# Kernel tuning notes

Measured on AMD Instinct MI355X. Metric: run time of the kernel, lower is better.

The kernel has to match this reference:

```python
import jax, jax.numpy as jnp
import numpy as np

N_HEAD = 16


def setup_inputs() -> dict:
    key = jax.random.key(0)
    k1, k2, k3 = jax.random.split(key, 3)
    B, T, C = 2, 2048, 1024
    x = jax.random.normal(k1, (B, T, C), dtype=jnp.float32)
    attention_mask = jnp.zeros((B, 1, 1, T), dtype=jnp.float32)
    W_attn = jax.random.normal(k2, (C, 3 * C), dtype=jnp.float32) * 0.02
    b_attn = jnp.zeros((3 * C,), dtype=jnp.float32)
    W_proj = jax.random.normal(k3, (C, C), dtype=jnp.float32) * 0.02
    b_proj = jnp.zeros((C,), dtype=jnp.float32)
    return {"x": x, "attention_mask": attention_mask, "W_attn": W_attn,
            "b_attn": b_attn, "W_proj": W_proj, "b_proj": b_proj}


def reference(x, attention_mask, W_attn, b_attn, W_proj, b_proj):
    B, T, C = x.shape
    H = N_HEAD
    d = C // H
    qkv = x @ W_attn + b_attn                      # [B, T, 3C]
    q, k, v = jnp.split(qkv, 3, axis=-1)
    q = q.reshape(B, T, H, d).transpose(0, 2, 1, 3)  # [B, H, T, d]
    k = k.reshape(B, T, H, d).transpose(0, 2, 1, 3)
    v = v.reshape(B, T, H, d).transpose(0, 2, 1, 3)
    att = jnp.einsum('bhtd,bhsd->bhts', q, k) * (1.0 / np.sqrt(d))
    causal = jnp.tril(jnp.ones((T, T), dtype=bool))
    att = jnp.where(causal[None, None], att, jnp.float32(-10000.0))
    att = att + attention_mask                     # additive broadcast mask
    att = jax.nn.softmax(att, axis=-1)             # dropout p=0.0 -> identity
    y = jnp.einsum('bhts,bhsd->bhtd', att, v)      # [B, H, T, d]
    y = y.transpose(0, 2, 1, 3).reshape(B, T, C)
    return y @ W_proj + b_proj
```

## Files before the change

### kernel.cpp

```cpp
#include <hip/hip_runtime.h>
#include <hip/hip_bf16.h>
#include <stdint.h>

#define BATCH 2
#define TT 2048
#define CC 1024
#define NH 16
#define HD 64

typedef __attribute__((ext_vector_type(8))) short short8;
typedef __attribute__((ext_vector_type(4))) short sh4;
typedef __attribute__((ext_vector_type(4))) float f32x4;

#define MFMA16 __builtin_amdgcn_mfma_f32_16x16x32_bf16

__device__ __forceinline__ short f2bf(float f) {
  union { float f; unsigned u; } x;
  x.f = f;
  unsigned r = x.u + 0x7FFFu + ((x.u >> 16) & 1u);
  return (short)(r >> 16);
}

__global__ __launch_bounds__(256) void cast_f32_bf16(
    const float* __restrict__ s, short* __restrict__ d, int n) {
  const int i = (blockIdx.x * 256 + threadIdx.x) * 8;
  if (i >= n) return;
  const float4 a = *reinterpret_cast<const float4*>(&s[i]);
  const float4 b = *reinterpret_cast<const float4*>(&s[i + 4]);
  short8 o;
  o[0] = f2bf(a.x); o[1] = f2bf(a.y); o[2] = f2bf(a.z); o[3] = f2bf(a.w);
  o[4] = f2bf(b.x); o[5] = f2bf(b.y); o[6] = f2bf(b.z); o[7] = f2bf(b.w);
  *reinterpret_cast<short8*>(&d[i]) = o;
}

__global__ __launch_bounds__(256) void transpose_cast_bf16(
    const float* __restrict__ W, short* __restrict__ Wt, int K, int N) {
  __shared__ __align__(16) float Ls[64][68];
  const int n0 = blockIdx.x * 64, k0 = blockIdx.y * 64;
  const int tid = threadIdx.x;
  {
    const int r = tid >> 4, c4 = (tid & 15) * 4;
#pragma unroll
    for (int p = 0; p < 4; ++p) {
      const float4 v = *reinterpret_cast<const float4*>(
          &W[(size_t)(k0 + r + p * 16) * N + n0 + c4]);
      *reinterpret_cast<float4*>(&Ls[r + p * 16][c4]) = v;
    }
  }
  __syncthreads();
  {
    const int n = tid >> 2;
    const int kk0 = (tid & 3) * 16;
#pragma unroll
    for (int half = 0; half < 2; ++half) {
      short8 o;
#pragma unroll
      for (int t = 0; t < 8; ++t) o[t] = f2bf(Ls[kk0 + half * 8 + t][n]);
      *reinterpret_cast<short8*>(&Wt[(size_t)(n0 + n) * K + k0 + kk0 + half * 8]) = o;
    }
  }
}

__global__ __launch_bounds__(256) void transpose_v(
    const short* __restrict__ qkv, short* __restrict__ vT) {
  __shared__ __align__(16) short Ls[64][72];
  const int s0 = blockIdx.x * 64;
  const int bh = blockIdx.y, b = bh >> 4, h = bh & 15;
  const int tid = threadIdx.x;
  const int r = tid >> 3, c = (tid & 7) * 8;
#pragma unroll
  for (int p = 0; p < 2; ++p) {
    *reinterpret_cast<short8*>(&Ls[r + p * 32][c]) =
        *reinterpret_cast<const short8*>(
            &qkv[(size_t)(b * TT + s0 + r + p * 32) * (3 * CC) + 2 * CC +
                 h * HD + c]);
  }
  __syncthreads();
  const int d = tid >> 2, ss = (tid & 3) * 16;
  short8 o0, o1;
#pragma unroll
  for (int t = 0; t < 8; ++t) { o0[t] = Ls[ss + t][d]; o1[t] = Ls[ss + 8 + t][d]; }
  short* dst = &vT[((size_t)(bh * HD + d)) * TT + s0 + ss];
  *reinterpret_cast<short8*>(dst) = o0;
  *reinterpret_cast<short8*>(dst + 8) = o1;
}

template <bool OUT_BF16>
__global__ __launch_bounds__(256) void gemm_bt_mfma(
    const short* __restrict__ A, const short* __restrict__ Bt,
    const float* __restrict__ bias, void* __restrict__ C, int M, int N, int K,
    int QS) {
  __shared__ __align__(16) short As[2 * 128 * 32];
  __shared__ __align__(16) short Bs[2 * 128 * 32];
  const int tid = threadIdx.x;
  const int w = tid >> 6, lane = tid & 63;
  const int quad = lane >> 4, l15 = lane & 15;
  const int m0 = blockIdx.y * 128, n0 = blockIdx.x * 128;
  const int wm = (w >> 1) * 64, wn = (w & 1) * 64;

  f32x4 acc[4][4] = {};
  const int row16 = lane >> 2;
  const int c4 = (lane & 3) * 8;

  for (int k0 = 0; k0 < K; k0 += 64) {
    __syncthreads();
#pragma unroll
    for (int p = 0; p < 2; ++p) {
      const int rbase = __builtin_amdgcn_readfirstlane((w * 2 + p) * 16);
#pragma unroll
      for (int kh = 0; kh < 2; ++kh) {
        const short* ga = &A[(size_t)(m0 + rbase + row16) * K + k0 + kh * 32 + c4];
        const short* gb = &Bt[(size_t)(n0 + rbase + row16) * K + k0 + kh * 32 + c4];
        __builtin_amdgcn_global_load_lds(
            (const __attribute__((address_space(1))) void*)ga,
            (__attribute__((address_space(3))) void*)&As[kh * 4096 + rbase * 32],
            16, 0, 0);
        __builtin_amdgcn_global_load_lds(
            (const __attribute__((address_space(1))) void*)gb,
            (__attribute__((address_space(3))) void*)&Bs[kh * 4096 + rbase * 32],
            16, 0, 0);
      }
    }
    __syncthreads();

    short8 af[2][4], bfr[2][4];
#pragma unroll
    for (int kh = 0; kh < 2; ++kh) {
#pragma unroll
      for (int i = 0; i < 4; ++i)
        af[kh][i] = *reinterpret_cast<const short8*>(
            &As[kh * 4096 + (wm + i * 16 + l15) * 32 + quad * 8]);
#pragma unroll
      for (int j = 0; j < 4; ++j)
        bfr[kh][j] = *reinterpret_cast<const short8*>(
            &Bs[kh * 4096 + (wn + j * 16 + l15) * 32 + quad * 8]);
    }
#pragma unroll
    for (int kh = 0; kh < 2; ++kh)
#pragma unroll
      for (int i = 0; i < 4; ++i)
#pragma unroll
        for (int j = 0; j < 4; ++j)
          acc[i][j] = MFMA16(af[kh][i], bfr[kh][j], acc[i][j], 0, 0, 0);
  }

#pragma unroll
  for (int i = 0; i < 4; ++i) {
#pragma unroll
    for (int r = 0; r < 4; ++r) {
      const int row = m0 + wm + i * 16 + quad * 4 + r;
#pragma unroll
      for (int j = 0; j < 4; ++j) {
        const int col = n0 + wn + j * 16 + l15;
        float v = acc[i][j][r] + bias[col];
        if (col < QS) v *= 0.125f;
        if (OUT_BF16)
          ((short*)C)[(size_t)row * N + col] = f2bf(v);
        else
          ((float*)C)[(size_t)row * N + col] = v;
      }
    }
  }
}

#define PST 72
__global__ __launch_bounds__(512) void attn_mfma5(
    const short* __restrict__ qkv, const short* __restrict__ vT,
    const float* __restrict__ mask, short* __restrict__ y) {
  __shared__ __align__(16) short Ks[2][64 * PST];
  __shared__ __align__(16) short Vs[2][64 * PST];
  __shared__ __align__(16) short Ps[128 * PST];
  const int tid = threadIdx.x;
  const int w = tid >> 6, lane = tid & 63;
  const int quad = lane >> 4, l15 = lane & 15;
  const int bh = blockIdx.y, b = bh >> 4, h = bh & 15;
  const int px = blockIdx.x;
  const int qh = 15 - px;
  const int nth = 2 * qh + 2;
  const int ntl = 2 * px + 2;
  const int ntot = nth + ntl;
  const int RS = 3 * CC;

  int qrow0 = qh * 128 + w * 16;

  short8 qf0, qf1;
  {
    const size_t qrow = (size_t)(b * TT + qrow0 + l15) * RS + h * HD + quad * 8;
    qf0 = *reinterpret_cast<const short8*>(&qkv[qrow]);
    qf1 = *reinterpret_cast<const short8*>(&qkv[qrow + 32]);
  }

  float l_run = 0.f;
  f32x4 o_acc[4] = {};

  const int sr = tid >> 3, sc = (tid & 7) * 8;
  const short* kbase = qkv + (size_t)(b * TT + sr) * RS + CC + h * HD + sc;
  const short* vbase = vT + (size_t)(bh * HD + sr) * TT + sc;
  const float* mptr = mask + b * TT + quad * 4;
  short* psrow = &Ps[(w * 16 + l15) * PST];
  const int kfo0 = quad * 8, kfo1 = 32 + quad * 8;

  short8 kpre = *reinterpret_cast<const short8*>(kbase);
  short8 vpre = *reinterpret_cast<const short8*>(vbase);

  for (int it = 0; it < ntot; ++it) {
    const int kt = (it >= nth) ? it - nth : it;
    const int s0 = kt * 64;

    if (it == nth) {
#pragma unroll
      for (int r = 0; r < 4; ++r) {
        const float lr = __shfl(l_run, quad * 4 + r, 64);
        const float inv = 1.0f / lr;
        const size_t row = (size_t)(b * TT + qrow0 + quad * 4 + r);
#pragma unroll
        for (int t = 0; t < 4; ++t)
          y[row * CC + h * HD + t * 16 + l15] = f2bf(o_acc[t][r] * inv);
      }
      qrow0 = px * 128 + w * 16;
      const size_t qrow = (size_t)(b * TT + qrow0 + l15) * RS + h * HD + quad * 8;
      qf0 = *reinterpret_cast<const short8*>(&qkv[qrow]);
      qf1 = *reinterpret_cast<const short8*>(&qkv[qrow + 32]);
      l_run = 0.f;
#pragma unroll
      for (int t = 0; t < 4; ++t) o_acc[t] = f32x4{0.f, 0.f, 0.f, 0.f};
    }

    const int cur = it & 1;
    *reinterpret_cast<short8*>(&Ks[cur][sr * PST + sc]) = kpre;
    *reinterpret_cast<short8*>(&Vs[cur][sr * PST + sc]) = vpre;
    __syncthreads();

    if (it + 1 < ntot) {
      const int ktn = (it + 1 == nth) ? 0 : kt + 1;
      kpre = *reinterpret_cast<const short8*>(kbase + (size_t)ktn * 64 * RS);
      vpre = *reinterpret_cast<const short8*>(vbase + ktn * 64);
    }

    if (s0 > qrow0 + 15) continue;

    f32x4 sa[4] = {};
#pragma unroll
    for (int j = 0; j < 4; ++j) {
      const short8 kf0 = *reinterpret_cast<const short8*>(
          &Ks[cur][(j * 16 + l15) * PST + kfo0]);
      const short8 kf1 = *reinterpret_cast<const short8*>(
          &Ks[cur][(j * 16 + l15) * PST + kfo1]);
      sa[j] = MFMA16(kf0, qf0, sa[j], 0, 0, 0);
      sa[j] = MFMA16(kf1, qf1, sa[j], 0, 0, 0);
    }

    f32x4 mv[4];
#pragma unroll
    for (int j = 0; j < 4; ++j)
      mv[j] = *reinterpret_cast<const f32x4*>(&mptr[s0 + j * 16]);

    float rs = 0.f;
    const bool boundary = (s0 + 63 > qrow0);
    const int qg = qrow0 + l15;
#pragma unroll
    for (int j = 0; j < 4; ++j) {
      sh4 pw;
#pragma unroll
      for (int r = 0; r < 4; ++r) {
        float v = sa[j][r] + mv[j][r];
        if (boundary) {
          const int sg = s0 + j * 16 + quad * 4 + r;
          if (sg > qg) v = -10000.0f;
        }
        const float p = __expf(v);
        union { float f; unsigned u; } pu;
        pu.f = p;
        pw[r] = (short)(pu.u >> 16);
        pu.u &= 0xffff0000u;
        rs += pu.f;
      }
      *reinterpret_cast<sh4*>(&psrow[j * 16 + quad * 4]) = pw;
    }
    rs += __shfl_xor(rs, 16, 64);
    rs += __shfl_xor(rs, 32, 64);
    l_run += rs;

    const short8 pf0 = *reinterpret_cast<const short8*>(&psrow[kfo0]);
    const short8 pf1 = *reinterpret_cast<const short8*>(&psrow[kfo1]);
#pragma unroll
    for (int t = 0; t < 4; ++t) {
      const short8 vf0 = *reinterpret_cast<const short8*>(
          &Vs[cur][(t * 16 + l15) * PST + kfo0]);
      const short8 vf1 = *reinterpret_cast<const short8*>(
          &Vs[cur][(t * 16 + l15) * PST + kfo1]);
      o_acc[t] = MFMA16(pf0, vf0, o_acc[t], 0, 0, 0);
      o_acc[t] = MFMA16(pf1, vf1, o_acc[t], 0, 0, 0);
    }
  }

#pragma unroll
  for (int r = 0; r < 4; ++r) {
    const float lr = __shfl(l_run, quad * 4 + r, 64);
    const float inv = 1.0f / lr;
    const size_t row = (size_t)(b * TT + qrow0 + quad * 4 + r);
#pragma unroll
    for (int t = 0; t < 4; ++t)
      y[row * CC + h * HD + t * 16 + l15] = f2bf(o_acc[t][r] * inv);
  }
}

extern "C" void kernel_launch(void* const* d_in, const int* in_sizes, int n_in,
                              void* d_out, int out_size, void* d_ws,
                              size_t ws_size, hipStream_t stream) {
  const float* x = (const float*)d_in[0];
  const float* attn_mask = (const float*)d_in[1];
  const float* W_attn = (const float*)d_in[2];
  const float* b_attn = (const float*)d_in[3];
  const float* W_proj = (const float*)d_in[4];
  const float* b_proj = (const float*)d_in[5];
  float* out = (float*)d_out;

  const int M = BATCH * TT;

  short* xb = (short*)d_ws;
  short* wat = xb + (size_t)M * CC;
  short* wpt = wat + (size_t)(3 * CC) * CC;
  short* qkvb = wpt + (size_t)CC * CC;
  short* yb = qkvb + (size_t)M * 3 * CC;
  short* vTb = yb + (size_t)M * CC;

  cast_f32_bf16<<<(M * CC) / (256 * 8), 256, 0, stream>>>(x, xb, M * CC);
  transpose_cast_bf16<<<dim3((3 * CC) / 64, CC / 64), 256, 0, stream>>>(
      W_attn, wat, CC, 3 * CC);
  transpose_cast_bf16<<<dim3(CC / 64, CC / 64), 256, 0, stream>>>(
      W_proj, wpt, CC, CC);

  gemm_bt_mfma<true><<<dim3((3 * CC) / 128, M / 128), 256, 0, stream>>>(
      xb, wat, b_attn, qkvb, M, 3 * CC, CC, CC);

  transpose_v<<<dim3(TT / 64, BATCH * NH), 256, 0, stream>>>(qkvb, vTb);

  attn_mfma5<<<dim3(8, BATCH * NH), 512, 0, stream>>>(
      qkvb, vTb, attn_mask, yb);

  gemm_bt_mfma<false><<<dim3(CC / 128, M / 128), 256, 0, stream>>>(
      yb, wpt, b_proj, out, M, CC, CC, 0);
}
```

Before: 217.9 us.

## Fuse prep casts into one kernel and shrink attention query tile to 64

The three preprocessing launches (x cast, W_attn and W_proj transpose-casts) are merged into one kernel that dispatches on block index, removing two launches. The attention kernel moves from 128-row query tiles with 8 waves to 64-row tiles with 4 waves, doubling grid size to 512 blocks while keeping the paired short/long causal tile balancing. Each thread now stages two K/V rows per tile, and the per-wave causal skip is dropped because every wave in a 64-row tile covers the diagonal. Smaller blocks improve occupancy and tail balance, but each K/V tile is now reused across fewer query rows.

```diff
diff --git a/kernel.cpp b/kernel.cpp
--- a/kernel.cpp
+++ b/kernel.cpp
@@ -21,23 +21,10 @@
   return (short)(r >> 16);
 }
 
-__global__ __launch_bounds__(256) void cast_f32_bf16(
-    const float* __restrict__ s, short* __restrict__ d, int n) {
-  const int i = (blockIdx.x * 256 + threadIdx.x) * 8;
-  if (i >= n) return;
-  const float4 a = *reinterpret_cast<const float4*>(&s[i]);
-  const float4 b = *reinterpret_cast<const float4*>(&s[i + 4]);
-  short8 o;
-  o[0] = f2bf(a.x); o[1] = f2bf(a.y); o[2] = f2bf(a.z); o[3] = f2bf(a.w);
-  o[4] = f2bf(b.x); o[5] = f2bf(b.y); o[6] = f2bf(b.z); o[7] = f2bf(b.w);
-  *reinterpret_cast<short8*>(&d[i]) = o;
-}
-
-__global__ __launch_bounds__(256) void transpose_cast_bf16(
-    const float* __restrict__ W, short* __restrict__ Wt, int K, int N) {
+__device__ __forceinline__ void transpose_cast_tile(
+    const float* __restrict__ W, short* __restrict__ Wt, int K, int N,
+    int n0, int k0, int tid) {
   __shared__ __align__(16) float Ls[64][68];
-  const int n0 = blockIdx.x * 64, k0 = blockIdx.y * 64;
-  const int tid = threadIdx.x;
   {
     const int r = tid >> 4, c4 = (tid & 15) * 4;
 #pragma unroll
@@ -58,6 +45,31 @@
       for (int t = 0; t < 8; ++t) o[t] = f2bf(Ls[kk0 + half * 8 + t][n]);
       *reinterpret_cast<short8*>(&Wt[(size_t)(n0 + n) * K + k0 + kk0 + half * 8]) = o;
     }
+  }
+}
+
+__global__ __launch_bounds__(256) void prep_fused(
+    const float* __restrict__ x, short* __restrict__ xb,
+    const float* __restrict__ W_attn, short* __restrict__ wat,
+    const float* __restrict__ W_proj, short* __restrict__ wpt) {
+  const int blk = blockIdx.x;
+  const int tid = threadIdx.x;
+  if (blk < 2048) {
+    const int i = (blk * 256 + tid) * 8;
+    const float4 a = *reinterpret_cast<const float4*>(&x[i]);
+    const float4 b = *reinterpret_cast<const float4*>(&x[i + 4]);
+    short8 o;
+    o[0] = f2bf(a.x); o[1] = f2bf(a.y); o[2] = f2bf(a.z); o[3] = f2bf(a.w);
+    o[4] = f2bf(b.x); o[5] = f2bf(b.y); o[6] = f2bf(b.z); o[7] = f2bf(b.w);
+    *reinterpret_cast<short8*>(&xb[i]) = o;
+  } else if (blk < 2816) {
+    const int b2 = blk - 2048;
+    transpose_cast_tile(W_attn, wat, CC, 3 * CC, (b2 % 48) * 64,
+                        (b2 / 48) * 64, tid);
+  } else {
+    const int b3 = blk - 2816;
+    transpose_cast_tile(W_proj, wpt, CC, CC, (b3 % 16) * 64, (b3 / 16) * 64,
+                        tid);
   }
 }
 
@@ -164,24 +176,24 @@
 }
 
 #define PST 72
-__global__ __launch_bounds__(512) void attn_mfma5(
+__global__ __launch_bounds__(256) void attn_mfma6(
     const short* __restrict__ qkv, const short* __restrict__ vT,
     const float* __restrict__ mask, short* __restrict__ y) {
   __shared__ __align__(16) short Ks[2][64 * PST];
   __shared__ __align__(16) short Vs[2][64 * PST];
-  __shared__ __align__(16) short Ps[128 * PST];
+  __shared__ __align__(16) short Ps[64 * PST];
   const int tid = threadIdx.x;
   const int w = tid >> 6, lane = tid & 63;
   const int quad = lane >> 4, l15 = lane & 15;
   const int bh = blockIdx.y, b = bh >> 4, h = bh & 15;
   const int px = blockIdx.x;
-  const int qh = 15 - px;
-  const int nth = 2 * qh + 2;
-  const int ntl = 2 * px + 2;
-  const int ntot = nth + ntl;
+  const int qh = 31 - px;
+  const int nth = qh + 1;
+  const int ntot = nth + px + 1;
   const int RS = 3 * CC;
 
-  int qrow0 = qh * 128 + w * 16;
+  int qt = qh;
+  int qrow0 = qt * 64 + w * 16;
 
   short8 qf0, qf1;
   {
@@ -200,11 +212,13 @@
   short* psrow = &Ps[(w * 16 + l15) * PST];
   const int kfo0 = quad * 8, kfo1 = 32 + quad * 8;
 
-  short8 kpre = *reinterpret_cast<const short8*>(kbase);
-  short8 vpre = *reinterpret_cast<const short8*>(vbase);
+  short8 kpre0 = *reinterpret_cast<const short8*>(kbase);
+  short8 kpre1 = *reinterpret_cast<const short8*>(kbase + (size_t)32 * RS);
+  short8 vpre0 = *reinterpret_cast<const short8*>(vbase);
+  short8 vpre1 = *reinterpret_cast<const short8*>(vbase + 32 * TT);
 
   for (int it = 0; it < ntot; ++it) {
-    const int kt = (it >= nth) ? it - nth : it;
+    const int kt = (it < nth) ? it : it - nth;
     const int s0 = kt * 64;
 
     if (it == nth) {
@@ -217,7 +231,8 @@
         for (int t = 0; t < 4; ++t)
           y[row * CC + h * HD + t * 16 + l15] = f2bf(o_acc[t][r] * inv);
       }
-      qrow0 = px * 128 + w * 16;
+      qt = px;
+      qrow0 = qt * 64 + w * 16;
       const size_t qrow = (size_t)(b * TT + qrow0 + l15) * RS + h * HD + quad * 8;
       qf0 = *reinterpret_cast<const short8*>(&qkv[qrow]);
       qf1 = *reinterpret_cast<const short8*>(&qkv[qrow + 32]);
@@ -227,17 +242,21 @@
     }
 
     const int cur = it & 1;
-    *reinterpret_cast<short8*>(&Ks[cur][sr * PST + sc]) = kpre;
-    *reinterpret_cast<short8*>(&Vs[cur][sr * PST + sc]) = vpre;
+    *reinterpret_cast<short8*>(&Ks[cur][sr * PST + sc]) = kpre0;
+    *reinterpret_cast<short8*>(&Ks[cur][(sr + 32) * PST + sc]) = kpre1;
+    *reinterpret_cast<short8*>(&Vs[cur][sr * PST + sc]) = vpre0;
+    *reinterpret_cast<short8*>(&Vs[cur][(sr + 32) * PST + sc]) = vpre1;
     __syncthreads();
 
     if (it + 1 < ntot) {
       const int ktn = (it + 1 == nth) ? 0 : kt + 1;
-      kpre = *reinterpret_cast<const short8*>(kbase + (size_t)ktn * 64 * RS);
-      vpre = *reinterpret_cast<const short8*>(vbase + ktn * 64);
-    }
-
-    if (s0 > qrow0 + 15) continue;
+      const short* kp = kbase + (size_t)ktn * 64 * RS;
+      const short* vp = vbase + ktn * 64;
+      kpre0 = *reinterpret_cast<const short8*>(kp);
+      kpre1 = *reinterpret_cast<const short8*>(kp + (size_t)32 * RS);
+      vpre0 = *reinterpret_cast<const short8*>(vp);
+      vpre1 = *reinterpret_cast<const short8*>(vp + 32 * TT);
+    }
 
     f32x4 sa[4] = {};
 #pragma unroll
@@ -256,7 +275,7 @@
       mv[j] = *reinterpret_cast<const f32x4*>(&mptr[s0 + j * 16]);
 
     float rs = 0.f;
-    const bool boundary = (s0 + 63 > qrow0);
+    const bool boundary = (kt == qt);
     const int qg = qrow0 + l15;
 #pragma unroll
     for (int j = 0; j < 4; ++j) {
@@ -325,18 +344,14 @@
   short* yb = qkvb + (size_t)M * 3 * CC;
   short* vTb = yb + (size_t)M * CC;
 
-  cast_f32_bf16<<<(M * CC) / (256 * 8), 256, 0, stream>>>(x, xb, M * CC);
-  transpose_cast_bf16<<<dim3((3 * CC) / 64, CC / 64), 256, 0, stream>>>(
-      W_attn, wat, CC, 3 * CC);
-  transpose_cast_bf16<<<dim3(CC / 64, CC / 64), 256, 0, stream>>>(
-      W_proj, wpt, CC, CC);
+  prep_fused<<<3072, 256, 0, stream>>>(x, xb, W_attn, wat, W_proj, wpt);
 
   gemm_bt_mfma<true><<<dim3((3 * CC) / 128, M / 128), 256, 0, stream>>>(
       xb, wat, b_attn, qkvb, M, 3 * CC, CC, CC);
 
   transpose_v<<<dim3(TT / 64, BATCH * NH), 256, 0, stream>>>(qkvb, vTb);
 
-  attn_mfma5<<<dim3(8, BATCH * NH), 512, 0, stream>>>(
+  attn_mfma6<<<dim3(16, BATCH * NH), 256, 0, stream>>>(
       qkvb, vTb, attn_mask, yb);
 
   gemm_bt_mfma<false><<<dim3(CC / 128, M / 128), 256, 0, stream>>>(
```

Result: faster. 207.4 us (-4.8%).
